# Kernel optimization log

Measured on AMD Instinct MI355X. Metric: run time of the kernel, lower is better.

The kernel has to match this reference:

```python
import jax, jax.numpy as jnp
import numpy as np

N, E, T, Q, G = 50000, 800000, 1000000, 1000000, 4096
L, H, D, HID, ED = 3, 8, 16, 128, 16
EPS = 1e-8


def setup_inputs() -> dict:
    key = jax.random.key(0)
    ks = jax.random.split(key, 20)
    inp = {
        "x": jax.random.normal(ks[0], (N, HID), jnp.float32),
        "pos": jax.random.normal(ks[1], (N, 3), jnp.float32),
        "edge_attr": jax.random.normal(ks[2], (E, ED), jnp.float32),
        "temps": jax.random.uniform(ks[3], (G, 1), jnp.float32),
        "edge_index": jax.random.randint(ks[4], (2, E), 0, N, jnp.int32),
        "triple_index": jax.random.randint(ks[5], (3, T), 0, N, jnp.int32),
        "quadra_index": jax.random.randint(ks[6], (4, Q), 0, N, jnp.int32),
        "batch": jnp.sort(jax.random.randint(ks[7], (N,), 0, G, jnp.int32)),
        "W": jax.random.normal(ks[8], (L, HID, HID), jnp.float32) * 0.08,
        "a_e": jax.random.normal(ks[9], (L, H, 2 * D + 1), jnp.float32) * 0.1,
        "a_t": jax.random.normal(ks[10], (L, H, 2 * D + 1), jnp.float32) * 0.1,
        "a_q": jax.random.normal(ks[11], (L, H, 2 * D + 1), jnp.float32) * 0.1,
        "We": jax.random.normal(ks[12], (L, ED, H), jnp.float32) * 0.1,
        "W1": jax.random.normal(ks[13], (2 * HID + 1, 256), jnp.float32) * 0.06,
        "b1": jnp.zeros((256,), jnp.float32),
        "W2": jax.random.normal(ks[14], (256, 256), jnp.float32) * 0.06,
        "b2": jnp.zeros((256,), jnp.float32),
        "W3": jax.random.normal(ks[15], (256, 1), jnp.float32) * 0.06,
        "b3": jnp.zeros((1,), jnp.float32),
    }
    return inp


def _seg_softmax(logits, seg, n):
    # numerically stable segment softmax over destination nodes
    m = jax.ops.segment_max(logits, seg, num_segments=n)
    m = jnp.where(jnp.isfinite(m), m, 0.0)
    e = jnp.exp(logits - m[seg])
    s = jax.ops.segment_sum(e, seg, num_segments=n)
    return e / (s[seg] + 1e-16)


def _hop(hh, src, dst, geom, a, bias=None):
    # hh: [N,H,D]; gather-attend-scatter for one interaction order
    q, k = hh[dst], hh[src]                      # [M,H,D]
    logits = jnp.einsum('mhd,hd->mh', q, a[:, :D]) \
           + jnp.einsum('mhd,hd->mh', k, a[:, D:2 * D]) \
           + geom[:, None] * a[:, 2 * D]
    if bias is not None:
        logits = logits + bias
    logits = jax.nn.leaky_relu(logits, 0.2)
    alpha = _seg_softmax(logits, dst, hh.shape[0])  # [M,H]
    return jax.ops.segment_sum(k * alpha[..., None], dst, num_segments=hh.shape[0])


def _geom_features(pos, edge_index, triple_index, quadra_index):
    # edge distance
    d = jnp.linalg.norm(pos[edge_index[0]] - pos[edge_index[1]] + EPS, axis=-1)
    # triple angle cos at center node j of (i,j,k)
    i, j, k = triple_index
    u, v = pos[i] - pos[j], pos[k] - pos[j]
    cos_a = (u * v).sum(-1) / (jnp.linalg.norm(u, axis=-1) * jnp.linalg.norm(v, axis=-1) + EPS)
    # quadra dihedral cos of (p0,p1,p2,p3)
    p0, p1, p2, p3 = pos[quadra_index[0]], pos[quadra_index[1]], pos[quadra_index[2]], pos[quadra_index[3]]
    b1, b2, b3 = p1 - p0, p2 - p1, p3 - p2
    n1, n2 = jnp.cross(b1, b2), jnp.cross(b2, b3)
    cos_d = (n1 * n2).sum(-1) / (jnp.linalg.norm(n1, axis=-1) * jnp.linalg.norm(n2, axis=-1) + EPS)
    return d, cos_a, cos_d


def reference(x, pos, edge_attr, temps, edge_index, triple_index, quadra_index, batch,
              W, a_e, a_t, a_q, We, W1, b1, W2, b2, W3, b3):
    d, cos_a, cos_d = _geom_features(pos, edge_index, triple_index, quadra_index)
    e_src, e_dst = edge_index[1], edge_index[0]
    t_src, t_dst = triple_index[2], triple_index[0]
    q_src, q_dst = quadra_index[3], quadra_index[0]
    h = x
    for l in range(L):
        hl = h @ W[l]                              # [N,HID]
        hh = hl.reshape(N, H, D)
        bias_e = edge_attr @ We[l]                 # [E,H]
        agg = _hop(hh, e_src, e_dst, d, a_e[l], bias_e) \
            + _hop(hh, t_src, t_dst, cos_a, a_t[l]) \
            + _hop(hh, q_src, q_dst, cos_d, a_q[l])
        h = jax.nn.elu(hl + agg.reshape(N, HID))
    # readout: sum + max pooling per graph, concat temperature scalar
    s = jax.ops.segment_sum(h, batch, num_segments=G)
    mx = jax.ops.segment_max(h, batch, num_segments=G)
    mx = jnp.where(jnp.isfinite(mx), mx, 0.0)
    mol = jnp.concatenate([s, mx, temps], axis=-1)  # [G, 2*HID+1]
    hdn = jax.nn.elu(mol @ W1 + b1)
    hdn = jax.nn.elu(hdn @ W2 + b2)
    return hdn @ W3 + b3
```

## Files before the change

### kernel.cpp

```cpp
#include <hip/hip_runtime.h>
#include <hip/hip_fp16.h>

#define NN 50000
#define EE 800000
#define TT 1000000
#define QQ 1000000
#define GG 4096
#define HID 128
#define NH 8
#define DH 16
#define CAPC 96

__device__ __forceinline__ float eluf(float x){ return x > 0.f ? x : expm1f(x); }

__global__ void k_count3(const int* __restrict__ ei, const int* __restrict__ ti, const int* __restrict__ qi,
                         int* __restrict__ cnt){
  int i = blockIdx.x*blockDim.x + threadIdx.x;
  if (i < EE) atomicAdd(&cnt[ei[i]], 1);
  else if (i < EE+TT) atomicAdd(&cnt[NN + ti[i-EE]], 1);
  else if (i < EE+TT+QQ) atomicAdd(&cnt[2*NN + qi[i-EE-TT]], 1);
}

__global__ __launch_bounds__(1024) void k_scan4(const int* __restrict__ cnt,
    int* __restrict__ off_e, int* __restrict__ off_t, int* __restrict__ off_q,
    int* __restrict__ cur_e, int* __restrict__ cur_t, int* __restrict__ cur_q,
    const int* __restrict__ batch, int* __restrict__ goff){
  int b = blockIdx.x, t = threadIdx.x;
  if (b == 3){
    for (int g=t; g<=GG; g+=1024){
      int lo=0, hi=NN;
      while (lo<hi){ int mid=(lo+hi)>>1; if (batch[mid]<g) lo=mid+1; else hi=mid; }
      goff[g]=lo;
    }
    return;
  }
  __shared__ int part[1024];
  const int* c = cnt + b*NN;
  int* off = (b==0)?off_e:(b==1)?off_t:off_q;
  int* cur = (b==0)?cur_e:(b==1)?cur_t:cur_q;
  int chunk = (NN + 1023) >> 10;
  int s0 = t*chunk, s1 = min(NN, s0+chunk);
  int sum = 0;
  for (int i=s0;i<s1;i++) sum += c[i];
  part[t] = sum;
  __syncthreads();
  for (int d=1; d<1024; d<<=1){
    int v = (t>=d) ? part[t-d] : 0;
    __syncthreads();
    part[t] += v;
    __syncthreads();
  }
  int run = (t==0) ? 0 : part[t-1];
  for (int i=s0;i<s1;i++){ off[i]=run; cur[i]=run; run += c[i]; }
  if (t==0) off[NN] = part[1023];
}

__global__ void k_fillgeom(const float* __restrict__ pos,
    const int* __restrict__ ei, const int* __restrict__ ti, const int* __restrict__ qi,
    int* __restrict__ cur_e, int* __restrict__ cur_t, int* __restrict__ cur_q,
    int* __restrict__ csrc_e, int* __restrict__ csrc_t, int* __restrict__ csrc_q,
    float* __restrict__ cg_e, float* __restrict__ cg_t, float* __restrict__ cg_q,
    int* __restrict__ epos_e){
  int i = blockIdx.x*blockDim.x + threadIdx.x;
  if (i < EE){
    int dn = ei[i], sn = ei[EE+i];
    float dx = pos[dn*3+0]-pos[sn*3+0]+1e-8f;
    float dy = pos[dn*3+1]-pos[sn*3+1]+1e-8f;
    float dz = pos[dn*3+2]-pos[sn*3+2]+1e-8f;
    float d = sqrtf(dx*dx+dy*dy+dz*dz);
    int p = atomicAdd(&cur_e[dn], 1);
    csrc_e[p] = sn; cg_e[p] = d; epos_e[i] = p;
  } else if (i < EE+TT){
    int m = i-EE;
    int a = ti[m], b = ti[TT+m], c = ti[2*TT+m];
    float ux = pos[a*3+0]-pos[b*3+0], uy = pos[a*3+1]-pos[b*3+1], uz = pos[a*3+2]-pos[b*3+2];
    float vx = pos[c*3+0]-pos[b*3+0], vy = pos[c*3+1]-pos[b*3+1], vz = pos[c*3+2]-pos[b*3+2];
    float num = ux*vx+uy*vy+uz*vz;
    float den = sqrtf(ux*ux+uy*uy+uz*uz)*sqrtf(vx*vx+vy*vy+vz*vz) + 1e-8f;
    int p = atomicAdd(&cur_t[a], 1);
    csrc_t[p] = c; cg_t[p] = num/den;
  } else if (i < EE+TT+QQ){
    int m = i-EE-TT;
    int p0 = qi[m], p1 = qi[QQ+m], p2 = qi[2*QQ+m], p3 = qi[3*QQ+m];
    float b1x = pos[p1*3+0]-pos[p0*3+0], b1y = pos[p1*3+1]-pos[p0*3+1], b1z = pos[p1*3+2]-pos[p0*3+2];
    float b2x = pos[p2*3+0]-pos[p1*3+0], b2y = pos[p2*3+1]-pos[p1*3+1], b2z = pos[p2*3+2]-pos[p1*3+2];
    float b3x = pos[p3*3+0]-pos[p2*3+0], b3y = pos[p3*3+1]-pos[p2*3+1], b3z = pos[p3*3+2]-pos[p2*3+2];
    float n1x = b1y*b2z - b1z*b2y, n1y = b1z*b2x - b1x*b2z, n1z = b1x*b2y - b1y*b2x;
    float n2x = b2y*b3z - b2z*b3y, n2y = b2z*b3x - b2x*b3z, n2z = b2x*b3y - b2y*b3x;
    float num = n1x*n2x+n1y*n2y+n1z*n2z;
    float den = sqrtf(n1x*n1x+n1y*n1y+n1z*n1z)*sqrtf(n2x*n2x+n2y*n2y+n2z*n2z) + 1e-8f;
    int p = atomicAdd(&cur_q[p0], 1);
    csrc_q[p] = p3; cg_q[p] = num/den;
  }
}

#define GR 16
__global__ __launch_bounds__(128) void k_gemm(const float* __restrict__ A, const float* __restrict__ W,
                                              float* __restrict__ B, __half* __restrict__ B16){
  int col = threadIdx.x;
  int r0 = blockIdx.x * GR;
  const float* Ab = A + (size_t)r0*HID;
  float acc[GR];
  #pragma unroll
  for (int r=0;r<GR;r++) acc[r]=0.f;
  #pragma unroll 4
  for (int k=0;k<HID;k++){
    float wv = W[k*HID+col];
    #pragma unroll
    for (int r=0;r<GR;r++) acc[r] = fmaf(Ab[r*HID+k], wv, acc[r]);
  }
  #pragma unroll
  for (int r=0;r<GR;r++){
    size_t oi = (size_t)(r0+r)*HID+col;
    B[oi] = acc[r];
    B16[oi] = __float2half(acc[r]);
  }
}

__global__ void k_projbias(const float* __restrict__ hl,
    const float* __restrict__ ae, const float* __restrict__ at, const float* __restrict__ aq,
    const float* __restrict__ ea, const float* __restrict__ Wel, const int* __restrict__ epos_e,
    float* __restrict__ qa_e, float* __restrict__ ka_e,
    float* __restrict__ qa_t, float* __restrict__ ka_t,
    float* __restrict__ qa_q, float* __restrict__ ka_q,
    float* __restrict__ biasP){
  int i = blockIdx.x*blockDim.x + threadIdx.x;
  if (i < NN*NH){
    int h = i & 7; int n = i >> 3;
    const float* v = hl + (size_t)n*HID + h*DH;
    float x[DH];
    #pragma unroll
    for (int d=0; d<DH; d++) x[d] = v[d];
    const float* Ae = ae + h*33; const float* At_ = at + h*33; const float* Aq = aq + h*33;
    float s0=0,s1=0,s2=0,s3=0,s4=0,s5=0;
    #pragma unroll
    for (int d=0; d<DH; d++){
      s0 = fmaf(x[d], Ae[d],      s0);  s1 = fmaf(x[d], Ae[DH+d],  s1);
      s2 = fmaf(x[d], At_[d],     s2);  s3 = fmaf(x[d], At_[DH+d], s3);
      s4 = fmaf(x[d], Aq[d],      s4);  s5 = fmaf(x[d], Aq[DH+d],  s5);
    }
    qa_e[i]=s0; ka_e[i]=s1; qa_t[i]=s2; ka_t[i]=s3; qa_q[i]=s4; ka_q[i]=s5;
  } else {
    int m = i - NN*NH;
    if (m < EE){
      float a[16];
      #pragma unroll
      for (int c=0;c<16;c++) a[c] = ea[(size_t)m*16+c];
      size_t p = (size_t)epos_e[m]*NH;
      #pragma unroll
      for (int h=0;h<NH;h++){
        float s = 0.f;
        #pragma unroll
        for (int c=0;c<16;c++) s = fmaf(a[c], Wel[c*NH+h], s);
        biasP[p+h] = s;
      }
    }
  }
}

__global__ __launch_bounds__(128) void k_hop3(
    const int* __restrict__ off_e, const int* __restrict__ off_t, const int* __restrict__ off_q,
    const int* __restrict__ csrc_e, const int* __restrict__ csrc_t, const int* __restrict__ csrc_q,
    const float* __restrict__ cg_e, const float* __restrict__ cg_t, const float* __restrict__ cg_q,
    const float* __restrict__ biasP,
    const float* __restrict__ qa_e, const float* __restrict__ ka_e,
    const float* __restrict__ qa_t, const float* __restrict__ ka_t,
    const float* __restrict__ qa_q, const float* __restrict__ ka_q,
    const float* __restrict__ ae, const float* __restrict__ at, const float* __restrict__ aq,
    const __half* __restrict__ hh16, const float* __restrict__ hlr, float* __restrict__ hout){
  __shared__ float sh_e[3][CAPC*NH];
  __shared__ int   sh_src[3][CAPC];
  __shared__ float sh_s[3*NH];
  __shared__ float sh_qa[3*NH];
  __shared__ float sh_coef[3*NH];
  int n = blockIdx.x, t = threadIdx.x;
  int w = t >> 6, l = t & 63;
  if (t < 24){
    int p = t>>3, h = t&7;
    const float* a  = (p==0)?ae:(p==1)?at:aq;
    const float* qa = (p==0)?qa_e:(p==1)?qa_t:qa_q;
    sh_coef[t] = a[h*33+32];
    sh_qa[t]   = qa[n*NH+h];
    sh_s[t]    = 0.f;
  }
  int st_e = off_e[n], de = off_e[n+1]-st_e;
  int st_t = off_t[n], dt = off_t[n+1]-st_t;
  int st_q = off_q[n], dq = off_q[n+1]-st_q;
  __syncthreads();
  float aE0=0,aE1=0,aT0=0,aT1=0,aQ0=0,aQ1=0;
  int h  = t & 7;
  int hg = l >> 3;
  int maxd = max(de, max(dt, dq));
  for (int base=0; base<maxd; base+=CAPC){
    int ce = min(CAPC, de-base); if (ce<0) ce=0;
    int ct = min(CAPC, dt-base); if (ct<0) ct=0;
    int cq = min(CAPC, dq-base); if (cq<0) cq=0;
    if (t < ce) sh_src[0][t] = csrc_e[st_e+base+t];
    if (t < ct) sh_src[1][t] = csrc_t[st_t+base+t];
    if (t < cq) sh_src[2][t] = csrc_q[st_q+base+t];
    __syncthreads();
    float dE=0.f, dT=0.f, dQ=0.f;
    for (int i=t; i<ce*NH; i+=128){
      int m = i>>3;
      float lg = sh_qa[h] + ka_e[sh_src[0][m]*NH+h] + cg_e[st_e+base+m]*sh_coef[h]
               + biasP[(size_t)(st_e+base)*NH + i];
      lg = lg>=0.f ? lg : 0.2f*lg;
      float e = __expf(lg);
      sh_e[0][i] = e; dE += e;
    }
    for (int i=t; i<ct*NH; i+=128){
      int m = i>>3;
      float lg = sh_qa[8+h] + ka_t[sh_src[1][m]*NH+h] + cg_t[st_t+base+m]*sh_coef[8+h];
      lg = lg>=0.f ? lg : 0.2f*lg;
      float e = __expf(lg);
      sh_e[1][i] = e; dT += e;
    }
    for (int i=t; i<cq*NH; i+=128){
      int m = i>>3;
      float lg = sh_qa[16+h] + ka_q[sh_src[2][m]*NH+h] + cg_q[st_q+base+m]*sh_coef[16+h];
      lg = lg>=0.f ? lg : 0.2f*lg;
      float e = __expf(lg);
      sh_e[2][i] = e; dQ += e;
    }
    dE += __shfl_xor(dE, 8); dE += __shfl_xor(dE, 16); dE += __shfl_xor(dE, 32);
    dT += __shfl_xor(dT, 8); dT += __shfl_xor(dT, 16); dT += __shfl_xor(dT, 32);
    dQ += __shfl_xor(dQ, 8); dQ += __shfl_xor(dQ, 16); dQ += __shfl_xor(dQ, 32);
    if (l < 8){
      atomicAdd(&sh_s[l], dE);
      atomicAdd(&sh_s[8+l], dT);
      atomicAdd(&sh_s[16+l], dQ);
    }
    __syncthreads();
    {
      int m = w;
      for (; m+4 <= ce; m += 4){
        int s0 = sh_src[0][m], s1 = sh_src[0][m+2];
        float a0 = sh_e[0][m*NH+hg], a1 = sh_e[0][(m+2)*NH+hg];
        float2 f0 = __half22float2(*(const __half2*)&hh16[(size_t)s0*HID + 2*l]);
        float2 f1 = __half22float2(*(const __half2*)&hh16[(size_t)s1*HID + 2*l]);
        aE0 = fmaf(f0.x, a0, aE0); aE1 = fmaf(f0.y, a0, aE1);
        aE0 = fmaf(f1.x, a1, aE0); aE1 = fmaf(f1.y, a1, aE1);
      }
      for (; m < ce; m += 2){
        int s0 = sh_src[0][m];
        float a0 = sh_e[0][m*NH+hg];
        float2 f0 = __half22float2(*(const __half2*)&hh16[(size_t)s0*HID + 2*l]);
        aE0 = fmaf(f0.x, a0, aE0); aE1 = fmaf(f0.y, a0, aE1);
      }
    }
    {
      int m = w;
      for (; m+4 <= ct; m += 4){
        int s0 = sh_src[1][m], s1 = sh_src[1][m+2];
        float a0 = sh_e[1][m*NH+hg], a1 = sh_e[1][(m+2)*NH+hg];
        float2 f0 = __half22float2(*(const __half2*)&hh16[(size_t)s0*HID + 2*l]);
        float2 f1 = __half22float2(*(const __half2*)&hh16[(size_t)s1*HID + 2*l]);
        aT0 = fmaf(f0.x, a0, aT0); aT1 = fmaf(f0.y, a0, aT1);
        aT0 = fmaf(f1.x, a1, aT0); aT1 = fmaf(f1.y, a1, aT1);
      }
      for (; m < ct; m += 2){
        int s0 = sh_src[1][m];
        float a0 = sh_e[1][m*NH+hg];
        float2 f0 = __half22float2(*(const __half2*)&hh16[(size_t)s0*HID + 2*l]);
        aT0 = fmaf(f0.x, a0, aT0); aT1 = fmaf(f0.y, a0, aT1);
      }
    }
    {
      int m = w;
      for (; m+4 <= cq; m += 4){
        int s0 = sh_src[2][m], s1 = sh_src[2][m+2];
        float a0 = sh_e[2][m*NH+hg], a1 = sh_e[2][(m+2)*NH+hg];
        float2 f0 = __half22float2(*(const __half2*)&hh16[(size_t)s0*HID + 2*l]);
        float2 f1 = __half22float2(*(const __half2*)&hh16[(size_t)s1*HID + 2*l]);
        aQ0 = fmaf(f0.x, a0, aQ0); aQ1 = fmaf(f0.y, a0, aQ1);
        aQ0 = fmaf(f1.x, a1, aQ0); aQ1 = fmaf(f1.y, a1, aQ1);
      }
      for (; m < cq; m += 2){
        int s0 = sh_src[2][m];
        float a0 = sh_e[2][m*NH+hg];
        float2 f0 = __half22float2(*(const __half2*)&hh16[(size_t)s0*HID + 2*l]);
        aQ0 = fmaf(f0.x, a0, aQ0); aQ1 = fmaf(f0.y, a0, aQ1);
      }
    }
    __syncthreads();
  }
  float* red = &sh_e[0][0];
  *(float2*)&red[(0*2+w)*128 + 2*l] = make_float2(aE0, aE1);
  *(float2*)&red[(1*2+w)*128 + 2*l] = make_float2(aT0, aT1);
  *(float2*)&red[(2*2+w)*128 + 2*l] = make_float2(aQ0, aQ1);
  __syncthreads();
  int ho = t >> 4;
  float outv = (red[t]       + red[128+t]) / (sh_s[ho]    + 1e-16f)
             + (red[256+t]   + red[384+t]) / (sh_s[8+ho]  + 1e-16f)
             + (red[512+t]   + red[640+t]) / (sh_s[16+ho] + 1e-16f);
  size_t oi = (size_t)n*HID + t;
  hout[oi] = eluf(hlr[oi] + outv);
}

__global__ __launch_bounds__(128) void k_pool(const float* __restrict__ h, const int* __restrict__ goff,
                                              float* __restrict__ gs, float* __restrict__ gmx){
  int g = blockIdx.x, t = threadIdx.x;
  int s = goff[g], e = goff[g+1];
  float sum = 0.f, mx = -INFINITY;
  for (int n=s; n<e; n++){
    float v = h[(size_t)n*HID+t];
    sum += v; mx = fmaxf(mx, v);
  }
  gs[(size_t)g*HID+t] = sum;
  gmx[(size_t)g*HID+t] = (s < e) ? mx : 0.f;
}

#define GPB 8
#define MSTR 260
__global__ __launch_bounds__(256) void k_mlp(const float* __restrict__ gs, const float* __restrict__ gmx,
    const float* __restrict__ temps,
    const float* __restrict__ W1, const float* __restrict__ b1,
    const float* __restrict__ W2, const float* __restrict__ b2,
    const float* __restrict__ W3, const float* __restrict__ b3,
    float* __restrict__ out){
  __shared__ float mol[GPB][MSTR];
  __shared__ float hd[GPB][MSTR];
  int g0 = blockIdx.x*GPB, t = threadIdx.x;
  for (int i=t; i<GPB*HID; i+=256){
    int g=i>>7, d=i&127;
    mol[g][d]     = gs[(size_t)(g0+g)*HID+d];
    mol[g][128+d] = gmx[(size_t)(g0+g)*HID+d];
  }
  if (t < GPB){ mol[t][256]=temps[g0+t]; mol[t][257]=0.f; mol[t][258]=0.f; mol[t][259]=0.f; }
  __syncthreads();
  float acc[GPB];
  #pragma unroll
  for (int g=0;g<GPB;g++) acc[g]=b1[t];
  for (int k0=0;k0<256;k0+=4){
    float w0=W1[(size_t)(k0+0)*256+t], w1=W1[(size_t)(k0+1)*256+t];
    float w2=W1[(size_t)(k0+2)*256+t], w3=W1[(size_t)(k0+3)*256+t];
    #pragma unroll
    for (int g=0;g<GPB;g++){
      float4 m4 = *(const float4*)&mol[g][k0];
      acc[g] = fmaf(m4.x,w0, fmaf(m4.y,w1, fmaf(m4.z,w2, fmaf(m4.w,w3, acc[g]))));
    }
  }
  { float wl=W1[(size_t)256*256+t];
    #pragma unroll
    for (int g=0;g<GPB;g++) acc[g]=fmaf(mol[g][256],wl,acc[g]); }
  #pragma unroll
  for (int g=0;g<GPB;g++) hd[g][t]=eluf(acc[g]);
  __syncthreads();
  #pragma unroll
  for (int g=0;g<GPB;g++) acc[g]=b2[t];
  for (int k0=0;k0<256;k0+=4){
    float w0=W2[(size_t)(k0+0)*256+t], w1=W2[(size_t)(k0+1)*256+t];
    float w2=W2[(size_t)(k0+2)*256+t], w3=W2[(size_t)(k0+3)*256+t];
    #pragma unroll
    for (int g=0;g<GPB;g++){
      float4 h4 = *(const float4*)&hd[g][k0];
      acc[g] = fmaf(h4.x,w0, fmaf(h4.y,w1, fmaf(h4.z,w2, fmaf(h4.w,w3, acc[g]))));
    }
  }
  float w3v = W3[t];
  #pragma unroll
  for (int g=0;g<GPB;g++) mol[g][t] = eluf(acc[g])*w3v;
  __syncthreads();
  int g = t >> 5, j = t & 31;
  float s = 0.f;
  for (int i=j; i<256; i+=32) s += mol[g][i];
  #pragma unroll
  for (int d=16; d>0; d>>=1) s += __shfl_down(s, d, 32);
  if (j == 0) out[g0+g] = s + b3[0];
}

extern "C" void kernel_launch(void* const* d_in, const int* in_sizes, int n_in,
                              void* d_out, int out_size, void* d_ws, size_t ws_size,
                              hipStream_t stream){
  const float* x         = (const float*)d_in[0];
  const float* pos       = (const float*)d_in[1];
  const float* edge_attr = (const float*)d_in[2];
  const float* temps     = (const float*)d_in[3];
  const int*   ei        = (const int*)d_in[4];
  const int*   ti        = (const int*)d_in[5];
  const int*   qi        = (const int*)d_in[6];
  const int*   batch     = (const int*)d_in[7];
  const float* W         = (const float*)d_in[8];
  const float* a_e       = (const float*)d_in[9];
  const float* a_t       = (const float*)d_in[10];
  const float* a_q       = (const float*)d_in[11];
  const float* We        = (const float*)d_in[12];
  const float* W1        = (const float*)d_in[13];
  const float* b1        = (const float*)d_in[14];
  const float* W2        = (const float*)d_in[15];
  const float* b2        = (const float*)d_in[16];
  const float* W3        = (const float*)d_in[17];
  const float* b3        = (const float*)d_in[18];
  float* out = (float*)d_out;

  char* base = (char*)d_ws; size_t woff = 0;
  auto alloc = [&](size_t bytes)->void*{
    void* p = base + woff;
    woff = (woff + bytes + 255) & ~(size_t)255;
    return p;
  };
  float*  hbuf   = (float*)alloc((size_t)NN*HID*4);
  float*  hl     = (float*)alloc((size_t)NN*HID*4);
  __half* hl16   = (__half*)alloc((size_t)NN*HID*2);
  float*  qa_e   = (float*)alloc((size_t)NN*NH*4);
  float*  ka_e   = (float*)alloc((size_t)NN*NH*4);
  float*  qa_t   = (float*)alloc((size_t)NN*NH*4);
  float*  ka_t   = (float*)alloc((size_t)NN*NH*4);
  float*  qa_q   = (float*)alloc((size_t)NN*NH*4);
  float*  ka_q   = (float*)alloc((size_t)NN*NH*4);
  int*    csrc_e = (int*)alloc((size_t)EE*4);
  int*    csrc_t = (int*)alloc((size_t)TT*4);
  int*    csrc_q = (int*)alloc((size_t)QQ*4);
  float*  cg_e   = (float*)alloc((size_t)EE*4);
  float*  cg_t   = (float*)alloc((size_t)TT*4);
  float*  cg_q   = (float*)alloc((size_t)QQ*4);
  float*  biasP  = (float*)alloc((size_t)EE*NH*4);
  int*    epos_e = (int*)alloc((size_t)EE*4);
  float*  gs     = (float*)alloc((size_t)GG*HID*4);
  float*  gmx    = (float*)alloc((size_t)GG*HID*4);
  int*    cnt    = (int*)alloc((size_t)3*NN*4);
  int*    off_e  = (int*)alloc((size_t)(NN+1)*4);
  int*    off_t  = (int*)alloc((size_t)(NN+1)*4);
  int*    off_q  = (int*)alloc((size_t)(NN+1)*4);
  int*    cur_e  = (int*)alloc((size_t)NN*4);
  int*    cur_t  = (int*)alloc((size_t)NN*4);
  int*    cur_q  = (int*)alloc((size_t)NN*4);
  int*    goff   = (int*)alloc((size_t)(GG+1)*4);

  hipMemsetAsync(cnt, 0, (size_t)3*NN*4, stream);
  int tot = EE+TT+QQ;
  k_count3<<<(tot+255)/256,256,0,stream>>>(ei, ti, qi, cnt);
  k_scan4<<<4,1024,0,stream>>>(cnt, off_e, off_t, off_q, cur_e, cur_t, cur_q, batch, goff);
  k_fillgeom<<<(tot+255)/256,256,0,stream>>>(pos, ei, ti, qi, cur_e, cur_t, cur_q,
                                             csrc_e, csrc_t, csrc_q, cg_e, cg_t, cg_q, epos_e);

  for (int l=0; l<3; l++){
    const float* hin = (l==0) ? x : hbuf;
    k_gemm<<<NN/GR,128,0,stream>>>(hin, W + (size_t)l*HID*HID, hl, hl16);
    k_projbias<<<(NN*NH+EE+255)/256,256,0,stream>>>(hl, a_e+l*264, a_t+l*264, a_q+l*264,
                                                    edge_attr, We + l*DH*NH, epos_e,
                                                    qa_e, ka_e, qa_t, ka_t, qa_q, ka_q, biasP);
    k_hop3<<<NN,128,0,stream>>>(off_e, off_t, off_q, csrc_e, csrc_t, csrc_q,
                                cg_e, cg_t, cg_q, biasP,
                                qa_e, ka_e, qa_t, ka_t, qa_q, ka_q,
                                a_e+l*264, a_t+l*264, a_q+l*264,
                                hl16, hl, hbuf);
  }

  k_pool<<<GG,128,0,stream>>>(hbuf, goff, gs, gmx);
  k_mlp<<<GG/GPB,256,0,stream>>>(gs, gmx, temps, W1, b1, W2, b2, W3, b3, out);
}
```

Measured before the change: 1.253 ms.

## Pack CSR source and geometry, pre-permute edge attributes, unroll gather deeper

Source index and geometry scalar are interleaved into one int2 array per hop, so each neighbor needs one load, and the geometry is staged in shared memory instead of being re-read per head. Edge attributes are permuted into CSR order once during setup, which removes the epos indirection and the scattered bias writes in every layer's projection kernel. The neighbor gather loop is factored into a helper unrolled to four loads in flight per iteration. In exchange there is one extra 51 MB permuted copy of the edge attributes at setup and some added shared memory and register pressure.

```diff
diff --git a/kernel.cpp b/kernel.cpp
--- a/kernel.cpp
+++ b/kernel.cpp
@@ -55,12 +55,11 @@
   if (t==0) off[NN] = part[1023];
 }
 
-__global__ void k_fillgeom(const float* __restrict__ pos,
+__global__ void k_fillgeom(const float* __restrict__ pos, const float* __restrict__ edge_attr,
     const int* __restrict__ ei, const int* __restrict__ ti, const int* __restrict__ qi,
     int* __restrict__ cur_e, int* __restrict__ cur_t, int* __restrict__ cur_q,
-    int* __restrict__ csrc_e, int* __restrict__ csrc_t, int* __restrict__ csrc_q,
-    float* __restrict__ cg_e, float* __restrict__ cg_t, float* __restrict__ cg_q,
-    int* __restrict__ epos_e){
+    int2* __restrict__ csg_e, int2* __restrict__ csg_t, int2* __restrict__ csg_q,
+    float* __restrict__ eaP){
   int i = blockIdx.x*blockDim.x + threadIdx.x;
   if (i < EE){
     int dn = ei[i], sn = ei[EE+i];
@@ -69,7 +68,10 @@
     float dz = pos[dn*3+2]-pos[sn*3+2]+1e-8f;
     float d = sqrtf(dx*dx+dy*dy+dz*dz);
     int p = atomicAdd(&cur_e[dn], 1);
-    csrc_e[p] = sn; cg_e[p] = d; epos_e[i] = p;
+    csg_e[p] = make_int2(sn, __float_as_int(d));
+    const float4* s = (const float4*)(edge_attr + (size_t)i*16);
+    float4* dst4 = (float4*)(eaP + (size_t)p*16);
+    dst4[0]=s[0]; dst4[1]=s[1]; dst4[2]=s[2]; dst4[3]=s[3];
   } else if (i < EE+TT){
     int m = i-EE;
     int a = ti[m], b = ti[TT+m], c = ti[2*TT+m];
@@ -78,7 +80,7 @@
     float num = ux*vx+uy*vy+uz*vz;
     float den = sqrtf(ux*ux+uy*uy+uz*uz)*sqrtf(vx*vx+vy*vy+vz*vz) + 1e-8f;
     int p = atomicAdd(&cur_t[a], 1);
-    csrc_t[p] = c; cg_t[p] = num/den;
+    csg_t[p] = make_int2(c, __float_as_int(num/den));
   } else if (i < EE+TT+QQ){
     int m = i-EE-TT;
     int p0 = qi[m], p1 = qi[QQ+m], p2 = qi[2*QQ+m], p3 = qi[3*QQ+m];
@@ -90,7 +92,7 @@
     float num = n1x*n2x+n1y*n2y+n1z*n2z;
     float den = sqrtf(n1x*n1x+n1y*n1y+n1z*n1z)*sqrtf(n2x*n2x+n2y*n2y+n2z*n2z) + 1e-8f;
     int p = atomicAdd(&cur_q[p0], 1);
-    csrc_q[p] = p3; cg_q[p] = num/den;
+    csg_q[p] = make_int2(p3, __float_as_int(num/den));
   }
 }
 
@@ -119,7 +121,7 @@
 
 __global__ void k_projbias(const float* __restrict__ hl,
     const float* __restrict__ ae, const float* __restrict__ at, const float* __restrict__ aq,
-    const float* __restrict__ ea, const float* __restrict__ Wel, const int* __restrict__ epos_e,
+    const float* __restrict__ eaP, const float* __restrict__ Wel,
     float* __restrict__ qa_e, float* __restrict__ ka_e,
     float* __restrict__ qa_t, float* __restrict__ ka_t,
     float* __restrict__ qa_q, float* __restrict__ ka_q,
@@ -144,9 +146,11 @@
     int m = i - NN*NH;
     if (m < EE){
       float a[16];
-      #pragma unroll
-      for (int c=0;c<16;c++) a[c] = ea[(size_t)m*16+c];
-      size_t p = (size_t)epos_e[m]*NH;
+      const float4* s4 = (const float4*)(eaP + (size_t)m*16);
+      float4 v0=s4[0], v1=s4[1], v2=s4[2], v3=s4[3];
+      a[0]=v0.x;a[1]=v0.y;a[2]=v0.z;a[3]=v0.w; a[4]=v1.x;a[5]=v1.y;a[6]=v1.z;a[7]=v1.w;
+      a[8]=v2.x;a[9]=v2.y;a[10]=v2.z;a[11]=v2.w; a[12]=v3.x;a[13]=v3.y;a[14]=v3.z;a[15]=v3.w;
+      size_t p = (size_t)m*NH;
       #pragma unroll
       for (int h=0;h<NH;h++){
         float s = 0.f;
@@ -158,10 +162,33 @@
   }
 }
 
+__device__ __forceinline__ void gather_acc(const __half* __restrict__ hh16,
+    const int* __restrict__ srcs, const float* __restrict__ es,
+    int cnt, int w, int hg, int l, float& a0, float& a1){
+  int m = w;
+  for (; m+8 <= cnt; m += 8){
+    int s0=srcs[m], s1=srcs[m+2], s2=srcs[m+4], s3=srcs[m+6];
+    float e0=es[m*NH+hg], e1=es[(m+2)*NH+hg], e2=es[(m+4)*NH+hg], e3=es[(m+6)*NH+hg];
+    float2 f0 = __half22float2(*(const __half2*)&hh16[(size_t)s0*HID + 2*l]);
+    float2 f1 = __half22float2(*(const __half2*)&hh16[(size_t)s1*HID + 2*l]);
+    float2 f2 = __half22float2(*(const __half2*)&hh16[(size_t)s2*HID + 2*l]);
+    float2 f3 = __half22float2(*(const __half2*)&hh16[(size_t)s3*HID + 2*l]);
+    a0 = fmaf(f0.x, e0, a0); a1 = fmaf(f0.y, e0, a1);
+    a0 = fmaf(f1.x, e1, a0); a1 = fmaf(f1.y, e1, a1);
+    a0 = fmaf(f2.x, e2, a0); a1 = fmaf(f2.y, e2, a1);
+    a0 = fmaf(f3.x, e3, a0); a1 = fmaf(f3.y, e3, a1);
+  }
+  for (; m < cnt; m += 2){
+    int s0 = srcs[m];
+    float e0 = es[m*NH+hg];
+    float2 f0 = __half22float2(*(const __half2*)&hh16[(size_t)s0*HID + 2*l]);
+    a0 = fmaf(f0.x, e0, a0); a1 = fmaf(f0.y, e0, a1);
+  }
+}
+
 __global__ __launch_bounds__(128) void k_hop3(
     const int* __restrict__ off_e, const int* __restrict__ off_t, const int* __restrict__ off_q,
-    const int* __restrict__ csrc_e, const int* __restrict__ csrc_t, const int* __restrict__ csrc_q,
-    const float* __restrict__ cg_e, const float* __restrict__ cg_t, const float* __restrict__ cg_q,
+    const int2* __restrict__ csg_e, const int2* __restrict__ csg_t, const int2* __restrict__ csg_q,
     const float* __restrict__ biasP,
     const float* __restrict__ qa_e, const float* __restrict__ ka_e,
     const float* __restrict__ qa_t, const float* __restrict__ ka_t,
@@ -170,6 +197,7 @@
     const __half* __restrict__ hh16, const float* __restrict__ hlr, float* __restrict__ hout){
   __shared__ float sh_e[3][CAPC*NH];
   __shared__ int   sh_src[3][CAPC];
+  __shared__ float sh_geom[3][CAPC];
   __shared__ float sh_s[3*NH];
   __shared__ float sh_qa[3*NH];
   __shared__ float sh_coef[3*NH];
@@ -195,14 +223,14 @@
     int ce = min(CAPC, de-base); if (ce<0) ce=0;
     int ct = min(CAPC, dt-base); if (ct<0) ct=0;
     int cq = min(CAPC, dq-base); if (cq<0) cq=0;
-    if (t < ce) sh_src[0][t] = csrc_e[st_e+base+t];
-    if (t < ct) sh_src[1][t] = csrc_t[st_t+base+t];
-    if (t < cq) sh_src[2][t] = csrc_q[st_q+base+t];
+    if (t < ce){ int2 v = csg_e[st_e+base+t]; sh_src[0][t]=v.x; sh_geom[0][t]=__int_as_float(v.y); }
+    if (t < ct){ int2 v = csg_t[st_t+base+t]; sh_src[1][t]=v.x; sh_geom[1][t]=__int_as_float(v.y); }
+    if (t < cq){ int2 v = csg_q[st_q+base+t]; sh_src[2][t]=v.x; sh_geom[2][t]=__int_as_float(v.y); }
     __syncthreads();
     float dE=0.f, dT=0.f, dQ=0.f;
     for (int i=t; i<ce*NH; i+=128){
       int m = i>>3;
-      float lg = sh_qa[h] + ka_e[sh_src[0][m]*NH+h] + cg_e[st_e+base+m]*sh_coef[h]
+      float lg = sh_qa[h] + ka_e[sh_src[0][m]*NH+h] + sh_geom[0][m]*sh_coef[h]
                + biasP[(size_t)(st_e+base)*NH + i];
       lg = lg>=0.f ? lg : 0.2f*lg;
       float e = __expf(lg);
@@ -210,14 +238,14 @@
     }
     for (int i=t; i<ct*NH; i+=128){
       int m = i>>3;
-      float lg = sh_qa[8+h] + ka_t[sh_src[1][m]*NH+h] + cg_t[st_t+base+m]*sh_coef[8+h];
+      float lg = sh_qa[8+h] + ka_t[sh_src[1][m]*NH+h] + sh_geom[1][m]*sh_coef[8+h];
       lg = lg>=0.f ? lg : 0.2f*lg;
       float e = __expf(lg);
       sh_e[1][i] = e; dT += e;
     }
     for (int i=t; i<cq*NH; i+=128){
       int m = i>>3;
-      float lg = sh_qa[16+h] + ka_q[sh_src[2][m]*NH+h] + cg_q[st_q+base+m]*sh_coef[16+h];
+      float lg = sh_qa[16+h] + ka_q[sh_src[2][m]*NH+h] + sh_geom[2][m]*sh_coef[16+h];
       lg = lg>=0.f ? lg : 0.2f*lg;
       float e = __expf(lg);
       sh_e[2][i] = e; dQ += e;
@@ -231,57 +259,9 @@
       atomicAdd(&sh_s[16+l], dQ);
     }
     __syncthreads();
-    {
-      int m = w;
-      for (; m+4 <= ce; m += 4){
-        int s0 = sh_src[0][m], s1 = sh_src[0][m+2];
-        float a0 = sh_e[0][m*NH+hg], a1 = sh_e[0][(m+2)*NH+hg];
-        float2 f0 = __half22float2(*(const __half2*)&hh16[(size_t)s0*HID + 2*l]);
-        float2 f1 = __half22float2(*(const __half2*)&hh16[(size_t)s1*HID + 2*l]);
-        aE0 = fmaf(f0.x, a0, aE0); aE1 = fmaf(f0.y, a0, aE1);
-        aE0 = fmaf(f1.x, a1, aE0); aE1 = fmaf(f1.y, a1, aE1);
-      }
-      for (; m < ce; m += 2){
-        int s0 = sh_src[0][m];
-        float a0 = sh_e[0][m*NH+hg];
-        float2 f0 = __half22float2(*(const __half2*)&hh16[(size_t)s0*HID + 2*l]);
-        aE0 = fmaf(f0.x, a0, aE0); aE1 = fmaf(f0.y, a0, aE1);
-      }
-    }
-    {
-      int m = w;
-      for (; m+4 <= ct; m += 4){
-        int s0 = sh_src[1][m], s1 = sh_src[1][m+2];
-        float a0 = sh_e[1][m*NH+hg], a1 = sh_e[1][(m+2)*NH+hg];
-        float2 f0 = __half22float2(*(const __half2*)&hh16[(size_t)s0*HID + 2*l]);
-        float2 f1 = __half22float2(*(const __half2*)&hh16[(size_t)s1*HID + 2*l]);
-        aT0 = fmaf(f0.x, a0, aT0); aT1 = fmaf(f0.y, a0, aT1);
-        aT0 = fmaf(f1.x, a1, aT0); aT1 = fmaf(f1.y, a1, aT1);
-      }
-      for (; m < ct; m += 2){
-        int s0 = sh_src[1][m];
-        float a0 = sh_e[1][m*NH+hg];
-        float2 f0 = __half22float2(*(const __half2*)&hh16[(size_t)s0*HID + 2*l]);
-        aT0 = fmaf(f0.x, a0, aT0); aT1 = fmaf(f0.y, a0, aT1);
-      }
-    }
-    {
-      int m = w;
-      for (; m+4 <= cq; m += 4){
-        int s0 = sh_src[2][m], s1 = sh_src[2][m+2];
-        float a0 = sh_e[2][m*NH+hg], a1 = sh_e[2][(m+2)*NH+hg];
-        float2 f0 = __half22float2(*(const __half2*)&hh16[(size_t)s0*HID + 2*l]);
-        float2 f1 = __half22float2(*(const __half2*)&hh16[(size_t)s1*HID + 2*l]);
-        aQ0 = fmaf(f0.x, a0, aQ0); aQ1 = fmaf(f0.y, a0, aQ1);
-        aQ0 = fmaf(f1.x, a1, aQ0); aQ1 = fmaf(f1.y, a1, aQ1);
-      }
-      for (; m < cq; m += 2){
-        int s0 = sh_src[2][m];
-        float a0 = sh_e[2][m*NH+hg];
-        float2 f0 = __half22float2(*(const __half2*)&hh16[(size_t)s0*HID + 2*l]);
-        aQ0 = fmaf(f0.x, a0, aQ0); aQ1 = fmaf(f0.y, a0, aQ1);
-      }
-    }
+    gather_acc(hh16, sh_src[0], sh_e[0], ce, w, hg, l, aE0, aE1);
+    gather_acc(hh16, sh_src[1], sh_e[1], ct, w, hg, l, aT0, aT1);
+    gather_acc(hh16, sh_src[2], sh_e[2], cq, w, hg, l, aQ0, aQ1);
     __syncthreads();
   }
   float* red = &sh_e[0][0];
@@ -408,14 +388,11 @@
   float*  ka_t   = (float*)alloc((size_t)NN*NH*4);
   float*  qa_q   = (float*)alloc((size_t)NN*NH*4);
   float*  ka_q   = (float*)alloc((size_t)NN*NH*4);
-  int*    csrc_e = (int*)alloc((size_t)EE*4);
-  int*    csrc_t = (int*)alloc((size_t)TT*4);
-  int*    csrc_q = (int*)alloc((size_t)QQ*4);
-  float*  cg_e   = (float*)alloc((size_t)EE*4);
-  float*  cg_t   = (float*)alloc((size_t)TT*4);
-  float*  cg_q   = (float*)alloc((size_t)QQ*4);
+  int2*   csg_e  = (int2*)alloc((size_t)EE*8);
+  int2*   csg_t  = (int2*)alloc((size_t)TT*8);
+  int2*   csg_q  = (int2*)alloc((size_t)QQ*8);
+  float*  eaP    = (float*)alloc((size_t)EE*16*4);
   float*  biasP  = (float*)alloc((size_t)EE*NH*4);
-  int*    epos_e = (int*)alloc((size_t)EE*4);
   float*  gs     = (float*)alloc((size_t)GG*HID*4);
   float*  gmx    = (float*)alloc((size_t)GG*HID*4);
   int*    cnt    = (int*)alloc((size_t)3*NN*4);
@@ -431,17 +408,16 @@
   int tot = EE+TT+QQ;
   k_count3<<<(tot+255)/256,256,0,stream>>>(ei, ti, qi, cnt);
   k_scan4<<<4,1024,0,stream>>>(cnt, off_e, off_t, off_q, cur_e, cur_t, cur_q, batch, goff);
-  k_fillgeom<<<(tot+255)/256,256,0,stream>>>(pos, ei, ti, qi, cur_e, cur_t, cur_q,
-                                             csrc_e, csrc_t, csrc_q, cg_e, cg_t, cg_q, epos_e);
+  k_fillgeom<<<(tot+255)/256,256,0,stream>>>(pos, edge_attr, ei, ti, qi, cur_e, cur_t, cur_q,
+                                             csg_e, csg_t, csg_q, eaP);
 
   for (int l=0; l<3; l++){
     const float* hin = (l==0) ? x : hbuf;
     k_gemm<<<NN/GR,128,0,stream>>>(hin, W + (size_t)l*HID*HID, hl, hl16);
     k_projbias<<<(NN*NH+EE+255)/256,256,0,stream>>>(hl, a_e+l*264, a_t+l*264, a_q+l*264,
-                                                    edge_attr, We + l*DH*NH, epos_e,
+                                                    eaP, We + l*DH*NH,
                                                     qa_e, ka_e, qa_t, ka_t, qa_q, ka_q, biasP);
-    k_hop3<<<NN,128,0,stream>>>(off_e, off_t, off_q, csrc_e, csrc_t, csrc_q,
-                                cg_e, cg_t, cg_q, biasP,
+    k_hop3<<<NN,128,0,stream>>>(off_e, off_t, off_q, csg_e, csg_t, csg_q, biasP,
                                 qa_e, ka_e, qa_t, ka_t, qa_q, ka_q,
                                 a_e+l*264, a_t+l*264, a_q+l*264,
                                 hl16, hl, hbuf);
```

Result: slower. 1.306 ms (+4.2%).
